# Kernel tuning notes

Hardware: AMD Instinct MI355X
Metric: run time of the kernel (lower is better)

Reference implementation:

```python
import jax, jax.numpy as jnp
import numpy as np

NUM_THING = 80
THING_STUFF_IDS = np.concatenate([np.arange(80), np.arange(80, 133)])  # thing_class_ids + stuff_class_ids
H_OUT, W_OUT = 641, 641
PIXEL_CONF_THR = 0.4
CLASS_CONF_THR = 0.7
NEG = -1e9  # mask value standing in for removing undetected slots


def _resize_bilinear_align_corners(x, h_out, w_out):
    # x: [h_in, w_in, C]; tf.compat.v1.image.resize_bilinear(..., align_corners=True)
    h_in, w_in = x.shape[0], x.shape[1]
    ys = jnp.linspace(0.0, h_in - 1.0, h_out)
    xs = jnp.linspace(0.0, w_in - 1.0, w_out)
    y0 = jnp.floor(ys).astype(jnp.int32)
    x0 = jnp.floor(xs).astype(jnp.int32)
    y1 = jnp.minimum(y0 + 1, h_in - 1)
    x1 = jnp.minimum(x0 + 1, w_in - 1)
    wy = (ys - y0.astype(ys.dtype))[:, None, None]
    wx = (xs - x0.astype(xs.dtype))[None, :, None]
    rows = x[y0] * (1.0 - wy) + x[y1] * wy          # [h_out, w_in, C]
    return rows[:, x0] * (1.0 - wx) + rows[:, x1] * wx  # [h_out, w_out, C]


def setup_inputs() -> dict:
    key = jax.random.key(0)
    k1, k2 = jax.random.split(key)
    pixel_space_mask_logits = jax.random.normal(k1, (161, 161, 128), dtype=jnp.float32)
    transformer_class_probs = jax.random.uniform(k2, (128, 134), dtype=jnp.float32)
    return {"pixel_space_mask_logits": pixel_space_mask_logits,
            "transformer_class_probs": transformer_class_probs}


def reference(pixel_space_mask_logits, transformer_class_probs):
    # --- _get_transformer_class_prediction (void channel dropped first) ---
    probs = transformer_class_probs[:, :-1]                     # [M, C]
    cls_pred = jnp.argmax(probs, axis=-1).astype(jnp.float32)   # [M]
    cls_conf = jnp.max(probs, axis=-1)                          # [M]
    detected = cls_conf >= CLASS_CONF_THR                       # [M] bool
    num_detections = jnp.sum(detected.astype(jnp.int32))
    # index of each detected slot within the detected subset (matches tf.gather order)
    det_subset_index = jnp.cumsum(detected.astype(jnp.int32)) - 1  # [M]

    # --- resize logits to full image (pieces=1 -> single full-width piece) ---
    resized = _resize_bilinear_align_corners(pixel_space_mask_logits, H_OUT, W_OUT)  # [H, W, M]

    # mask out undetected slots instead of gathering (same math, static shape)
    masked = jnp.where(detected[None, None, :], resized, NEG)   # [H, W, M]

    full_max = jnp.max(resized, axis=-1)                        # [H, W]
    det_max = jnp.max(masked, axis=-1)                          # [H, W]
    detected_pixel = (full_max == det_max).astype(jnp.float32)

    pixel_conf = jnp.max(jax.nn.softmax(masked, axis=-1), axis=-1)
    confident_region = (pixel_conf > PIXEL_CONF_THR).astype(jnp.float32) * detected_pixel

    argmax_slot = jnp.argmax(masked, axis=-1)                   # [H, W] slot index
    mask_id_map = det_subset_index[argmax_slot]                 # index within detected subset
    sem_float = cls_pred[argmax_slot]                           # detected_mask_class_pred gathered

    thing_mask = (sem_float < NUM_THING).astype(jnp.float32) * confident_region
    stuff_mask = (sem_float >= NUM_THING).astype(jnp.float32) * confident_region
    semantic_map = jnp.asarray(THING_STUFF_IDS, jnp.int32)[jnp.round(sem_float).astype(jnp.int32)]
    mask_id_map_plus_one = mask_id_map.astype(jnp.int32) + 1

    # --- empty-detection branch (tf.cond) expressed as select ---
    has_det = num_detections > 0
    mask_id_map_plus_one = jnp.where(has_det, mask_id_map_plus_one, jnp.ones_like(mask_id_map_plus_one))
    semantic_map = jnp.where(has_det, semantic_map, jnp.zeros_like(semantic_map))
    thing_mask = jnp.where(has_det, thing_mask, jnp.zeros_like(thing_mask))
    stuff_mask = jnp.where(has_det, stuff_mask, jnp.zeros_like(stuff_mask))
    return (mask_id_map_plus_one, semantic_map, thing_mask, stuff_mask)
```

## Files before the change

kernel.cpp:

```cpp
#include <hip/hip_runtime.h>

#pragma clang fp contract(off)

#define NP 410881

__global__ __launch_bounds__(1024) void slot_kernel(
    const float* __restrict__ probs, float* __restrict__ cls_pred,
    int* __restrict__ det_idx, unsigned long long* __restrict__ det_mask,
    int* __restrict__ num_det) {
  __shared__ float s_val[128];
  __shared__ int s_arg[128];
  __shared__ int s_tot0;
  int tid = threadIdx.x;
  int wv = tid >> 6, lane = tid & 63;

  float bvv[8];
  int bii[8];
#pragma unroll
  for (int k = 0; k < 8; ++k) {
    int r = wv * 8 + k;
    const float* row = probs + r * 134;
    float v0 = row[lane];
    float v1 = row[lane + 64];
    float v2 = (lane < 5) ? row[lane + 128] : -1.0f;
    float bv = v0;
    int bi = lane;
    if (v1 > bv) { bv = v1; bi = lane + 64; }
    if (v2 > bv) { bv = v2; bi = lane + 128; }
    bvv[k] = bv; bii[k] = bi;
  }
#pragma unroll
  for (int k = 0; k < 8; ++k) {
    float bv = bvv[k];
    int bi = bii[k];
#pragma unroll
    for (int off = 32; off; off >>= 1) {
      float ov = __shfl_xor(bv, off);
      int oi = __shfl_xor(bi, off);
      if (ov > bv || (ov == bv && oi < bi)) { bv = ov; bi = oi; }
    }
    if (lane == 0) { s_val[wv * 8 + k] = bv; s_arg[wv * 8 + k] = bi; }
  }
  __syncthreads();

  bool flag = false;
  unsigned long long b = 0;
  if (tid < 128) flag = s_val[tid] >= 0.7f;
  if (wv < 2) b = __ballot(flag);
  if (tid < 128 && lane == 0) {
    det_mask[wv] = b;
    if (wv == 0) s_tot0 = __popcll(b);
  }
  __syncthreads();
  if (tid < 128) {
    int incl = __popcll(b & ((1ull << lane) - 1)) + (flag ? 1 : 0) +
               (wv ? s_tot0 : 0);
    det_idx[tid] = incl - 1;
    cls_pred[tid] = (float)s_arg[tid];
    if (tid == 127) *num_det = incl;
  }
}

__global__ __launch_bounds__(512) void post_kernel(
    const float* __restrict__ logits, const float* __restrict__ ws_cls,
    const int* __restrict__ ws_didx,
    const unsigned long long* __restrict__ ws_mask,
    const int* __restrict__ ws_ndet, float* __restrict__ out) {
#pragma clang fp contract(off)
  __shared__ float sm[256], sT[256], srm[256];
  __shared__ int sa[256];

  int t = threadIdx.x;
  int p = t & 255;
  int half = t >> 8;
  int X0 = blockIdx.x << 4, Y0 = blockIdx.y << 4;
  int x = X0 + (p & 15);
  int y = Y0 + (p >> 4);
  bool valid = (x < 641) && (y < 641);
  int xc = min(x, 640), yc = min(y, 640);

  int ndet = *ws_ndet;
  if (ndet == 0) {
    if (valid && half == 0) {
      int i0 = y * 641 + x;
      out[i0] = 1.0f; out[NP + i0] = 0.f; out[2 * NP + i0] = 0.f; out[3 * NP + i0] = 0.f;
    }
    return;
  }

  int tx0 = xc >> 2, ty0 = yc >> 2;
  int tx1 = min(tx0 + 1, 160), ty1 = min(ty0 + 1, 160);
  float wx = 0.25f * (float)(xc & 3), iwx = 1.0f - wx;
  float wy = 0.25f * (float)(yc & 3), iwy = 1.0f - wy;

  int co = half << 6;
  const float* P00 = logits + ((ty0 * 161 + tx0) << 7) + co;
  const float* P01 = logits + ((ty0 * 161 + tx1) << 7) + co;
  const float* P10 = logits + ((ty1 * 161 + tx0) << 7) + co;
  const float* P11 = logits + ((ty1 * 161 + tx1) << 7) + co;

  float m = -INFINITY;
  int am = 0;
  float T = 0.f;
  float rm = -INFINITY;

  if (ndet == 128) {
    float ms[4], Ts[4];
    int as[4];
#pragma unroll
    for (int j = 0; j < 4; ++j) { ms[j] = -INFINITY; Ts[j] = 0.f; as[j] = 0; }
#define CH(A00, A01, A10, A11, CIDX, J)                                        \
  {                                                                            \
    float r0 = (A00) * iwy + (A10) * wy;                                       \
    float r1 = (A01) * iwy + (A11) * wy;                                       \
    float v = r0 * iwx + r1 * wx;                                              \
    bool g = v > ms[J]; ms[J] = g ? v : ms[J]; as[J] = g ? (CIDX) : as[J];     \
    Ts[J] += __expf(v);                                                        \
  }
#pragma unroll 2
    for (int c = 0; c < 64; c += 4) {
      float4 q00 = *(const float4*)(P00 + c);
      float4 q01 = *(const float4*)(P01 + c);
      float4 q10 = *(const float4*)(P10 + c);
      float4 q11 = *(const float4*)(P11 + c);
      CH(q00.x, q01.x, q10.x, q11.x, co + c + 0, 0);
      CH(q00.y, q01.y, q10.y, q11.y, co + c + 1, 1);
      CH(q00.z, q01.z, q10.z, q11.z, co + c + 2, 2);
      CH(q00.w, q01.w, q10.w, q11.w, co + c + 3, 3);
    }
#undef CH
    m = ms[0]; am = as[0];
#pragma unroll
    for (int j = 1; j < 4; ++j)
      if (ms[j] > m || (ms[j] == m && as[j] < am)) { m = ms[j]; am = as[j]; }
    T = (Ts[0] + Ts[1]) + (Ts[2] + Ts[3]);
    rm = m;
  } else {
    unsigned long long msk = ws_mask[half];
#pragma unroll 4
    for (int c = 0; c < 64; ++c) {
      float a00 = P00[c], a01 = P01[c];
      float a10 = P10[c], a11 = P11[c];
      float r0 = a00 * iwy + a10 * wy;
      float r1 = a01 * iwy + a11 * wy;
      float v = r0 * iwx + r1 * wx;
      rm = fmaxf(rm, v);
      if ((msk >> c) & 1) {
        bool g = v > m; m = g ? v : m; am = g ? (co + c) : am;
        T += __expf(v);
      }
    }
  }

  if (half == 1) { sm[p] = m; sa[p] = am; sT[p] = T; srm[p] = rm; }
  __syncthreads();
  if (half == 0) {
    float m1 = sm[p], T1 = sT[p], rm1 = srm[p];
    int a1 = sa[p];
    if (m1 > m || (m1 == m && a1 < am)) { m = m1; am = a1; }
    T += T1;
    rm = fmaxf(rm, rm1);
    bool dp = (rm == m);

    float cg = ((__expf(m) > 0.4f * T) && dp) ? 1.0f : 0.0f;
    float sem = ws_cls[am];
    float mid = (float)(ws_didx[am] + 1);
    float th = (sem < 80.f) ? cg : 0.f;
    float st = cg - th;
    if (valid) {
      int i0 = y * 641 + x;
      out[i0] = mid; out[NP + i0] = sem; out[2 * NP + i0] = th; out[3 * NP + i0] = st;
    }
  }
}

extern "C" void kernel_launch(void* const* d_in, const int* in_sizes, int n_in,
                              void* d_out, int out_size, void* d_ws,
                              size_t ws_size, hipStream_t stream) {
  const float* logits = (const float*)d_in[0];
  const float* probs = (const float*)d_in[1];
  float* out = (float*)d_out;

  float* ws_f = (float*)d_ws;
  float* cls_pred = ws_f;
  int* det_idx = (int*)(ws_f + 128);
  unsigned long long* det_mask = (unsigned long long*)(ws_f + 256);
  int* num_det = (int*)(ws_f + 260);

  slot_kernel<<<1, 1024, 0, stream>>>(probs, cls_pred, det_idx, det_mask,
                                      num_det);

  dim3 grid(41, 41);
  post_kernel<<<grid, 512, 0, stream>>>(logits, cls_pred, det_idx, det_mask,
                                        num_det, out);
}
```

Measured before the change: 97.50 us.

## Fuse slot classification into the pixel kernel and compute two pixels per thread

```diff
diff --git a/kernel.cpp b/kernel.cpp
--- a/kernel.cpp
+++ b/kernel.cpp
@@ -4,93 +4,94 @@
 
 #define NP 410881
 
-__global__ __launch_bounds__(1024) void slot_kernel(
-    const float* __restrict__ probs, float* __restrict__ cls_pred,
-    int* __restrict__ det_idx, unsigned long long* __restrict__ det_mask,
-    int* __restrict__ num_det) {
-  __shared__ float s_val[128];
-  __shared__ int s_arg[128];
-  __shared__ int s_tot0;
-  int tid = threadIdx.x;
-  int wv = tid >> 6, lane = tid & 63;
-
-  float bvv[8];
-  int bii[8];
+__global__ __launch_bounds__(512) void fused_kernel(
+    const float* __restrict__ logits, const float* __restrict__ probs,
+    float* __restrict__ out) {
+#pragma clang fp contract(off)
+  __shared__ float s_rv[128];
+  __shared__ int s_ra[128];
+  __shared__ float s_cls[128];
+  __shared__ int s_didx[128];
+  __shared__ unsigned long long s_mask[2];
+  __shared__ int s_ndet;
+  __shared__ float sAm[256], sAT[256], sArm[256];
+  __shared__ float sBm[256], sBT[256], sBrm[256];
+  __shared__ int sAa[256], sBa[256];
+
+  int bid = blockIdx.x;
+  int lin = (bid & 7) * 108 + (bid >> 3);
+  if (lin >= 861) return;
+  int by = lin / 21, bx = lin - by * 21;
+
+  int t = threadIdx.x;
+
+  {
+    int r = t >> 2, q = t & 3;
+    int j0 = q * 34;
+    int j1 = min(j0 + 34, 133);
+    const float* row = probs + r * 134;
+    float bv = -1.0f;
+    int bi = j0;
+    for (int j = j0; j < j1; ++j) {
+      float p = row[j];
+      if (p > bv) { bv = p; bi = j; }
+    }
 #pragma unroll
-  for (int k = 0; k < 8; ++k) {
-    int r = wv * 8 + k;
-    const float* row = probs + r * 134;
-    float v0 = row[lane];
-    float v1 = row[lane + 64];
-    float v2 = (lane < 5) ? row[lane + 128] : -1.0f;
-    float bv = v0;
-    int bi = lane;
-    if (v1 > bv) { bv = v1; bi = lane + 64; }
-    if (v2 > bv) { bv = v2; bi = lane + 128; }
-    bvv[k] = bv; bii[k] = bi;
-  }
-#pragma unroll
-  for (int k = 0; k < 8; ++k) {
-    float bv = bvv[k];
-    int bi = bii[k];
-#pragma unroll
-    for (int off = 32; off; off >>= 1) {
+    for (int off = 1; off <= 2; off <<= 1) {
       float ov = __shfl_xor(bv, off);
       int oi = __shfl_xor(bi, off);
       if (ov > bv || (ov == bv && oi < bi)) { bv = ov; bi = oi; }
     }
-    if (lane == 0) { s_val[wv * 8 + k] = bv; s_arg[wv * 8 + k] = bi; }
+    if (q == 0) { s_rv[r] = bv; s_ra[r] = bi; }
   }
   __syncthreads();
-
-  bool flag = false;
-  unsigned long long b = 0;
-  if (tid < 128) flag = s_val[tid] >= 0.7f;
-  if (wv < 2) b = __ballot(flag);
-  if (tid < 128 && lane == 0) {
-    det_mask[wv] = b;
-    if (wv == 0) s_tot0 = __popcll(b);
+  {
+    int wv = t >> 6, lane = t & 63;
+    bool flag = false;
+    if (t < 128) {
+      flag = (s_rv[t] >= 0.7f);
+      unsigned long long b = __ballot(flag);
+      if (lane == 0) s_mask[wv] = b;
+    }
+    __syncthreads();
+    if (t < 128) {
+      unsigned long long b = s_mask[wv];
+      int incl = __popcll(b & ((1ull << lane) - 1)) + (flag ? 1 : 0) +
+                 ((t >= 64) ? __popcll(s_mask[0]) : 0);
+      s_didx[t] = incl - 1;
+      s_cls[t] = (float)s_ra[t];
+      if (t == 127) s_ndet = incl;
+    }
   }
   __syncthreads();
-  if (tid < 128) {
-    int incl = __popcll(b & ((1ull << lane) - 1)) + (flag ? 1 : 0) +
-               (wv ? s_tot0 : 0);
-    det_idx[tid] = incl - 1;
-    cls_pred[tid] = (float)s_arg[tid];
-    if (tid == 127) *num_det = incl;
-  }
-}
-
-__global__ __launch_bounds__(512) void post_kernel(
-    const float* __restrict__ logits, const float* __restrict__ ws_cls,
-    const int* __restrict__ ws_didx,
-    const unsigned long long* __restrict__ ws_mask,
-    const int* __restrict__ ws_ndet, float* __restrict__ out) {
-#pragma clang fp contract(off)
-  __shared__ float sm[256], sT[256], srm[256];
-  __shared__ int sa[256];
-
-  int t = threadIdx.x;
-  int p = t & 255;
-  int half = t >> 8;
-  int X0 = blockIdx.x << 4, Y0 = blockIdx.y << 4;
-  int x = X0 + (p & 15);
-  int y = Y0 + (p >> 4);
-  bool valid = (x < 641) && (y < 641);
-  int xc = min(x, 640), yc = min(y, 640);
-
-  int ndet = *ws_ndet;
+
+  int p = t & 255, half = t >> 8;
+  int sx = p & 15, sy = p >> 4;
+  int x0 = (bx << 5) + (sx << 1);
+  int y = (by << 4) + sy;
+  int x0c = min(x0, 640), x1c = min(x0 + 1, 640), yc = min(y, 640);
+  bool vA = (x0 <= 640) && (y <= 640);
+  bool vB = (x0 + 1 <= 640) && (y <= 640);
+
+  int ndet = s_ndet;
   if (ndet == 0) {
-    if (valid && half == 0) {
-      int i0 = y * 641 + x;
-      out[i0] = 1.0f; out[NP + i0] = 0.f; out[2 * NP + i0] = 0.f; out[3 * NP + i0] = 0.f;
+    if (half == 0 && y <= 640) {
+      if (vA) {
+        int i = y * 641 + x0;
+        out[i] = 1.0f; out[NP + i] = 0.f; out[2 * NP + i] = 0.f; out[3 * NP + i] = 0.f;
+      }
+      if (vB) {
+        int i = y * 641 + x0 + 1;
+        out[i] = 1.0f; out[NP + i] = 0.f; out[2 * NP + i] = 0.f; out[3 * NP + i] = 0.f;
+      }
     }
     return;
   }
 
-  int tx0 = xc >> 2, ty0 = yc >> 2;
+  int tx0 = x0c >> 2, ty0 = yc >> 2;
   int tx1 = min(tx0 + 1, 160), ty1 = min(ty0 + 1, 160);
-  float wx = 0.25f * (float)(xc & 3), iwx = 1.0f - wx;
+  float wx0 = 0.25f * (float)(x0c & 3), iwx0 = 1.0f - wx0;
+  float wx1 = 0.25f * (float)(x1c & 3), iwx1 = 1.0f - wx1;
   float wy = 0.25f * (float)(yc & 3), iwy = 1.0f - wy;
 
   int co = half << 6;
@@ -99,77 +100,106 @@
   const float* P10 = logits + ((ty1 * 161 + tx0) << 7) + co;
   const float* P11 = logits + ((ty1 * 161 + tx1) << 7) + co;
 
-  float m = -INFINITY;
-  int am = 0;
-  float T = 0.f;
-  float rm = -INFINITY;
+  float mA = -INFINITY, mB = -INFINITY;
+  int aA = 0, aB = 0;
+  float TA = 0.f, TB = 0.f;
+  float rmA = -INFINITY, rmB = -INFINITY;
 
   if (ndet == 128) {
-    float ms[4], Ts[4];
-    int as[4];
+    float msA[2], msB[2], TsA[2], TsB[2];
+    int asA[2], asB[2];
 #pragma unroll
-    for (int j = 0; j < 4; ++j) { ms[j] = -INFINITY; Ts[j] = 0.f; as[j] = 0; }
+    for (int j = 0; j < 2; ++j) {
+      msA[j] = -INFINITY; msB[j] = -INFINITY;
+      TsA[j] = 0.f; TsB[j] = 0.f; asA[j] = 0; asB[j] = 0;
+    }
 #define CH(A00, A01, A10, A11, CIDX, J)                                        \
   {                                                                            \
     float r0 = (A00) * iwy + (A10) * wy;                                       \
     float r1 = (A01) * iwy + (A11) * wy;                                       \
-    float v = r0 * iwx + r1 * wx;                                              \
-    bool g = v > ms[J]; ms[J] = g ? v : ms[J]; as[J] = g ? (CIDX) : as[J];     \
-    Ts[J] += __expf(v);                                                        \
-  }
-#pragma unroll 2
+    float vva = r0 * iwx0 + r1 * wx0;                                          \
+    float vvb = r0 * iwx1 + r1 * wx1;                                          \
+    bool ga = vva > msA[J]; msA[J] = ga ? vva : msA[J]; asA[J] = ga ? (CIDX) : asA[J]; \
+    bool gb = vvb > msB[J]; msB[J] = gb ? vvb : msB[J]; asB[J] = gb ? (CIDX) : asB[J]; \
+    TsA[J] += __expf(vva);                                                     \
+    TsB[J] += __expf(vvb);                                                     \
+  }
+    float4 n00 = *(const float4*)(P00);
+    float4 n01 = *(const float4*)(P01);
+    float4 n10 = *(const float4*)(P10);
+    float4 n11 = *(const float4*)(P11);
+#pragma unroll 4
     for (int c = 0; c < 64; c += 4) {
-      float4 q00 = *(const float4*)(P00 + c);
-      float4 q01 = *(const float4*)(P01 + c);
-      float4 q10 = *(const float4*)(P10 + c);
-      float4 q11 = *(const float4*)(P11 + c);
+      float4 q00 = n00, q01 = n01, q10 = n10, q11 = n11;
+      if (c + 4 < 64) {
+        n00 = *(const float4*)(P00 + c + 4);
+        n01 = *(const float4*)(P01 + c + 4);
+        n10 = *(const float4*)(P10 + c + 4);
+        n11 = *(const float4*)(P11 + c + 4);
+      }
       CH(q00.x, q01.x, q10.x, q11.x, co + c + 0, 0);
       CH(q00.y, q01.y, q10.y, q11.y, co + c + 1, 1);
-      CH(q00.z, q01.z, q10.z, q11.z, co + c + 2, 2);
-      CH(q00.w, q01.w, q10.w, q11.w, co + c + 3, 3);
+      CH(q00.z, q01.z, q10.z, q11.z, co + c + 2, 0);
+      CH(q00.w, q01.w, q10.w, q11.w, co + c + 3, 1);
     }
 #undef CH
-    m = ms[0]; am = as[0];
-#pragma unroll
-    for (int j = 1; j < 4; ++j)
-      if (ms[j] > m || (ms[j] == m && as[j] < am)) { m = ms[j]; am = as[j]; }
-    T = (Ts[0] + Ts[1]) + (Ts[2] + Ts[3]);
-    rm = m;
+    mA = msA[0]; aA = asA[0]; mB = msB[0]; aB = asB[0];
+    if (msA[1] > mA || (msA[1] == mA && asA[1] < aA)) { mA = msA[1]; aA = asA[1]; }
+    if (msB[1] > mB || (msB[1] == mB && asB[1] < aB)) { mB = msB[1]; aB = asB[1]; }
+    TA = TsA[0] + TsA[1];
+    TB = TsB[0] + TsB[1];
+    rmA = mA; rmB = mB;
   } else {
-    unsigned long long msk = ws_mask[half];
+    unsigned long long msk = s_mask[half];
 #pragma unroll 4
     for (int c = 0; c < 64; ++c) {
       float a00 = P00[c], a01 = P01[c];
       float a10 = P10[c], a11 = P11[c];
       float r0 = a00 * iwy + a10 * wy;
       float r1 = a01 * iwy + a11 * wy;
-      float v = r0 * iwx + r1 * wx;
-      rm = fmaxf(rm, v);
+      float vva = r0 * iwx0 + r1 * wx0;
+      float vvb = r0 * iwx1 + r1 * wx1;
+      rmA = fmaxf(rmA, vva);
+      rmB = fmaxf(rmB, vvb);
       if ((msk >> c) & 1) {
-        bool g = v > m; m = g ? v : m; am = g ? (co + c) : am;
-        T += __expf(v);
-      }
-    }
-  }
-
-  if (half == 1) { sm[p] = m; sa[p] = am; sT[p] = T; srm[p] = rm; }
+        bool ga = vva > mA; mA = ga ? vva : mA; aA = ga ? (co + c) : aA;
+        bool gb = vvb > mB; mB = gb ? vvb : mB; aB = gb ? (co + c) : aB;
+        TA += __expf(vva);
+        TB += __expf(vvb);
+      }
+    }
+  }
+
+  if (half == 1) {
+    sAm[p] = mA; sAa[p] = aA; sAT[p] = TA; sArm[p] = rmA;
+    sBm[p] = mB; sBa[p] = aB; sBT[p] = TB; sBrm[p] = rmB;
+  }
   __syncthreads();
   if (half == 0) {
-    float m1 = sm[p], T1 = sT[p], rm1 = srm[p];
-    int a1 = sa[p];
-    if (m1 > m || (m1 == m && a1 < am)) { m = m1; am = a1; }
-    T += T1;
-    rm = fmaxf(rm, rm1);
-    bool dp = (rm == m);
-
-    float cg = ((__expf(m) > 0.4f * T) && dp) ? 1.0f : 0.0f;
-    float sem = ws_cls[am];
-    float mid = (float)(ws_didx[am] + 1);
-    float th = (sem < 80.f) ? cg : 0.f;
-    float st = cg - th;
-    if (valid) {
-      int i0 = y * 641 + x;
-      out[i0] = mid; out[NP + i0] = sem; out[2 * NP + i0] = th; out[3 * NP + i0] = st;
+    float hm = sAm[p]; int ha = sAa[p];
+    if (hm > mA) { mA = hm; aA = ha; }
+    TA += sAT[p];
+    rmA = fmaxf(rmA, sArm[p]);
+    hm = sBm[p]; ha = sBa[p];
+    if (hm > mB) { mB = hm; aB = ha; }
+    TB += sBT[p];
+    rmB = fmaxf(rmB, sBrm[p]);
+    bool dpA = (rmA == mA), dpB = (rmB == mB);
+
+    float cgA = ((__expf(mA) > 0.4f * TA) && dpA) ? 1.0f : 0.0f;
+    float cgB = ((__expf(mB) > 0.4f * TB) && dpB) ? 1.0f : 0.0f;
+    float semA = s_cls[aA], semB = s_cls[aB];
+    float midA = (float)(s_didx[aA] + 1), midB = (float)(s_didx[aB] + 1);
+    float thA = (semA < 80.f) ? cgA : 0.f, stA = cgA - thA;
+    float thB = (semB < 80.f) ? cgB : 0.f, stB = cgB - thB;
+
+    if (vA) {
+      int i = y * 641 + x0;
+      out[i] = midA; out[NP + i] = semA; out[2 * NP + i] = thA; out[3 * NP + i] = stA;
+    }
+    if (vB) {
+      int i = y * 641 + x0 + 1;
+      out[i] = midB; out[NP + i] = semB; out[2 * NP + i] = thB; out[3 * NP + i] = stB;
     }
   }
 }
@@ -181,16 +211,5 @@
   const float* probs = (const float*)d_in[1];
   float* out = (float*)d_out;
 
-  float* ws_f = (float*)d_ws;
-  float* cls_pred = ws_f;
-  int* det_idx = (int*)(ws_f + 128);
-  unsigned long long* det_mask = (unsigned long long*)(ws_f + 256);
-  int* num_det = (int*)(ws_f + 260);
-
-  slot_kernel<<<1, 1024, 0, stream>>>(probs, cls_pred, det_idx, det_mask,
-                                      num_det);
-
-  dim3 grid(41, 41);
-  post_kernel<<<grid, 512, 0, stream>>>(logits, cls_pred, det_idx, det_mask,
-                                        num_det, out);
+  fused_kernel<<<864, 512, 0, stream>>>(logits, probs, out);
 }
```

New measurement: 147.0 us. 50.8% more time.
